# Performance work log

Measured on AMD Instinct MI355X. Metric: run time of the kernel, lower is better.

Reference implementation:

```python
import math
import jax, jax.numpy as jnp
import numpy as np

B, T, N, D, H = 4, 12, 512, 256, 8


def _xavier(key, shape):
    limit = math.sqrt(6.0 / (shape[0] + shape[1]))
    return jax.random.uniform(key, shape, jnp.float32, -limit, limit)


def setup_inputs() -> dict:
    key = jax.random.key(0)
    kx, ks, kq, kk, kv, ko = jax.random.split(key, 6)
    return {
        "x": jax.random.normal(kx, (B, T, N, D), jnp.float32),
        "sim": jax.random.normal(ks, (N, N), jnp.float32),
        "Wq": _xavier(kq, (D, D)),
        "Wk": _xavier(kk, (D, D)),
        "Wv": _xavier(kv, (D, D)),
        "Wo": _xavier(ko, (D, D)),
    }


def reference(x, sim, Wq, Wk, Wv, Wo):
    # x: [B, T, N, D]; attention over spatial dim N, per (batch, time, head).
    b, t, n, d = x.shape
    hd = d // H
    scale = 1.0 / math.sqrt(hd)

    def split_heads(z):  # [B,T,N,D] -> [B,H,T,N,hd]
        return z.reshape(b, t, n, H, hd).transpose(0, 3, 1, 2, 4)

    q = split_heads(x @ Wq)
    k = split_heads(x @ Wk)
    v = split_heads(x @ Wv)

    # scores: [B,H,T,N,N]; additive sim bias broadcast over B,H,T
    scores = jnp.einsum("bhtnd,bhtmd->bhtnm", q, k) * scale + sim
    attn = jax.nn.softmax(scores, axis=-1)  # (dropout p=0.1 omitted: eval mode)
    out = jnp.einsum("bhtnm,bhtmd->bhtnd", attn, v)
    out = out.transpose(0, 2, 3, 1, 4).reshape(b, t, n, d)  # merge heads
    return out @ Wo
```

## Files before the change

### kernel.cpp

```cpp
#include <hip/hip_runtime.h>
#include <hip/hip_bf16.h>

#define BTT 48
#define SEQ 512
#define DIM 256
#define NH  8
#define HD  32
#define QKVD 768

typedef unsigned short u16;
typedef __attribute__((ext_vector_type(8))) short bf16x8;
typedef __attribute__((ext_vector_type(4))) float f32x4;
typedef __attribute__((ext_vector_type(2))) unsigned int u32x2;

__device__ __forceinline__ float fexp2(float x) {
#if __has_builtin(__builtin_amdgcn_exp2f)
  return __builtin_amdgcn_exp2f(x);
#else
  float r; asm("v_exp_f32 %0, %1" : "=v"(r) : "v"(x)); return r;
#endif
}
__device__ __forceinline__ unsigned cvtpk_bf16(float lo, float hi) {
  unsigned r;
  asm("v_cvt_pk_bf16_f32 %0, %1, %2" : "=v"(r) : "v"(lo), "v"(hi));
  return r;
}

__device__ __forceinline__ u16 f2b(float f) {
  __hip_bfloat16 h = __float2bfloat16(f);
  union { __hip_bfloat16 h; u16 u; } c; c.h = h; return c.u;
}
__device__ __forceinline__ bf16x8 ldfrag8(const u16* p) {
  union { uint2 u[2]; bf16x8 v; } f;
  f.u[0] = *reinterpret_cast<const uint2*>(p);
  f.u[1] = *reinterpret_cast<const uint2*>(p + 4);
  return f.v;
}
__device__ __forceinline__ bf16x8 ldfrag16(const u16* p) {
  union { uint4 u; bf16x8 v; } f;
  f.u = *reinterpret_cast<const uint4*>(p);
  return f.v;
}

__global__ __launch_bounds__(256) void wtcvt4_kernel(const float* __restrict__ W0,
                                                     const float* __restrict__ W1,
                                                     const float* __restrict__ W2,
                                                     const float* __restrict__ W3,
                                                     u16* __restrict__ dst, float sc0) {
  __shared__ float Ls[64][65];
  const int z = blockIdx.z;
  const float* W = (z == 0) ? W0 : (z == 1) ? W1 : (z == 2) ? W2 : W3;
  u16* Bt = dst + (size_t)z * DIM * DIM;
  const float sc = (z == 0) ? sc0 : 1.0f;
  const int t = threadIdx.x;
  const int kt = blockIdx.x * 64, nt = blockIdx.y * 64;
#pragma unroll
  for (int it = 0; it < 4; ++it) {
    int r = (t >> 4) + it * 16;
    int c = (t & 15) * 4;
    float4 v = *reinterpret_cast<const float4*>(&W[(size_t)(kt + r) * 256 + nt + c]);
    Ls[r][c] = v.x; Ls[r][c + 1] = v.y; Ls[r][c + 2] = v.z; Ls[r][c + 3] = v.w;
  }
  __syncthreads();
  const int n = t >> 2, kc = (t & 3) * 16;
  union { uint4 u[2]; u16 s[16]; } ob;
#pragma unroll
  for (int j = 0; j < 16; ++j) ob.s[j] = f2b(Ls[kc + j][n] * sc);
  u16* dp = Bt + (size_t)(nt + n) * 256 + kt + kc;
  *reinterpret_cast<uint4*>(dp)     = ob.u[0];
  *reinterpret_cast<uint4*>(dp + 8) = ob.u[1];
}

__global__ __launch_bounds__(256) void simpack_kernel(const float* __restrict__ sim,
                                                      float* __restrict__ simT2) {
  const float LOG2E = 1.4426950408889634f;
  int gid = blockIdx.x * 256 + threadIdx.x;
  int q = gid & 511, k4 = gid >> 9;
  float4 v = *reinterpret_cast<const float4*>(&sim[(size_t)q * 512 + k4 * 4]);
  v.x *= LOG2E; v.y *= LOG2E; v.z *= LOG2E; v.w *= LOG2E;
  *reinterpret_cast<float4*>(&simT2[((size_t)k4 * 512 + q) * 4]) = v;
}

template <typename AIN, typename OUT>
__global__ __launch_bounds__(256) void gemm_mfma(const AIN* __restrict__ A,
                                                 const u16* __restrict__ Bt,
                                                 OUT* __restrict__ C,
                                                 int M, int N, int K) {
  __shared__ u16 As[128][36];
  __shared__ u16 Bs[128][36];
  const int t = threadIdx.x, lane = t & 63, w = t >> 6;
  const int g = lane >> 4, ln = lane & 15;
  const int bm = blockIdx.x * 128, bn = blockIdx.y * 128;
  const int wr = (w & 1) * 64, wc = (w >> 1) * 64;
  const f32x4 zf = {0.f, 0.f, 0.f, 0.f};
  f32x4 acc[4][4];
#pragma unroll
  for (int i = 0; i < 4; ++i)
#pragma unroll
    for (int j = 0; j < 4; ++j) acc[i][j] = zf;

  const int r0 = t >> 2, c8 = (t & 3) * 8;
  uint4 bpre[2];
  float4 apf0[2], apf1[2];
  uint4 apb[2];
#pragma unroll
  for (int p = 0; p < 2; ++p) {
    const size_t arow = (size_t)(bm + r0 + p * 64) * K + c8;
    if constexpr (sizeof(AIN) == 4) {
      apf0[p] = *reinterpret_cast<const float4*>((const float*)A + arow);
      apf1[p] = *reinterpret_cast<const float4*>((const float*)A + arow + 4);
    } else {
      apb[p] = *reinterpret_cast<const uint4*>((const u16*)A + arow);
    }
    bpre[p] = *reinterpret_cast<const uint4*>(&Bt[(size_t)(bn + r0 + p * 64) * K + c8]);
  }

  for (int k0 = 0; k0 < K; k0 += 32) {
#pragma unroll
    for (int p = 0; p < 2; ++p) {
      const int r = r0 + p * 64;
      uint2 a0, a1;
      if constexpr (sizeof(AIN) == 4) {
        a0.x = cvtpk_bf16(apf0[p].x, apf0[p].y);
        a0.y = cvtpk_bf16(apf0[p].z, apf0[p].w);
        a1.x = cvtpk_bf16(apf1[p].x, apf1[p].y);
        a1.y = cvtpk_bf16(apf1[p].z, apf1[p].w);
      } else {
        union { uint4 u4; uint2 u2[2]; } av; av.u4 = apb[p];
        a0 = av.u2[0]; a1 = av.u2[1];
      }
      union { uint4 u4; uint2 u2[2]; } bv; bv.u4 = bpre[p];
      *reinterpret_cast<uint2*>(&As[r][c8])     = a0;
      *reinterpret_cast<uint2*>(&As[r][c8 + 4]) = a1;
      *reinterpret_cast<uint2*>(&Bs[r][c8])     = bv.u2[0];
      *reinterpret_cast<uint2*>(&Bs[r][c8 + 4]) = bv.u2[1];
    }
    if (k0 + 32 < K) {
#pragma unroll
      for (int p = 0; p < 2; ++p) {
        const size_t arow = (size_t)(bm + r0 + p * 64) * K + k0 + 32 + c8;
        if constexpr (sizeof(AIN) == 4) {
          apf0[p] = *reinterpret_cast<const float4*>((const float*)A + arow);
          apf1[p] = *reinterpret_cast<const float4*>((const float*)A + arow + 4);
        } else {
          apb[p] = *reinterpret_cast<const uint4*>((const u16*)A + arow);
        }
        bpre[p] = *reinterpret_cast<const uint4*>(&Bt[(size_t)(bn + r0 + p * 64) * K + k0 + 32 + c8]);
      }
    }
    __syncthreads();
    bf16x8 af[4], bfr[4];
#pragma unroll
    for (int i = 0; i < 4; ++i) af[i]  = ldfrag8(&As[wr + i * 16 + ln][g * 8]);
#pragma unroll
    for (int j = 0; j < 4; ++j) bfr[j] = ldfrag8(&Bs[wc + j * 16 + ln][g * 8]);
#pragma unroll
    for (int i = 0; i < 4; ++i)
#pragma unroll
      for (int j = 0; j < 4; ++j)
        acc[i][j] = __builtin_amdgcn_mfma_f32_16x16x32_bf16(af[i], bfr[j], acc[i][j], 0, 0, 0);
    __syncthreads();
  }
#pragma unroll
  for (int i = 0; i < 4; ++i)
#pragma unroll
    for (int j = 0; j < 4; ++j)
#pragma unroll
      for (int r = 0; r < 4; ++r) {
        const int row = bm + wr + i * 16 + g * 4 + r;
        const int col = bn + wc + j * 16 + ln;
        if constexpr (sizeof(OUT) == 2)
          ((u16*)C)[(size_t)row * N + col] = f2b(acc[i][j][r]);
        else
          ((float*)C)[(size_t)row * N + col] = acc[i][j][r];
      }
}

#define TRRD(dst, base, OFFSTR) \
  asm volatile("ds_read_b64_tr_b16 %0, %1 offset:" OFFSTR : "=v"(dst) : "v"(base))

__global__ __launch_bounds__(256) void attn_mfma10(const u16* __restrict__ QKV,
                                                   const float* __restrict__ simT2,
                                                   u16* __restrict__ O) {
  __shared__ u16 Ks[64][36];
  __shared__ u16 Vn[2][64][16];
  __shared__ u16 Pws[4][2][16][68];

  const int t = threadIdx.x;
  const int lane = t & 63, w = t >> 6;
  const int g = lane >> 4, ln = lane & 15;

  const int flat = blockIdx.x + 4 * (blockIdx.y + 8 * (int)blockIdx.z);
  const int work = (flat & 7) * 192 + (flat >> 3);
  const int qb = work & 3;
  const int grp = work >> 2;
  const int h = grp & 7, bt = grp >> 3;

  const size_t base = (size_t)bt * SEQ * QKVD + (size_t)h * HD;
  const u16* Qp = QKV + base;
  const u16* Kp = QKV + base + 256;
  const u16* Vp = QKV + base + 512;
  const size_t baseo = (size_t)bt * SEQ * DIM + (size_t)h * HD;
  const int wq = qb * 128 + w * 32;

  bf16x8 qf[2];
#pragma unroll
  for (int qt = 0; qt < 2; ++qt)
    qf[qt] = ldfrag16(&Qp[(size_t)(wq + qt * 16 + ln) * QKVD + g * 8]);

  const f32x4 zf = {0.f, 0.f, 0.f, 0.f};
  f32x4 o[2][2];
  float lacc[2];
#pragma unroll
  for (int qt = 0; qt < 2; ++qt) { o[qt][0] = zf; o[qt][1] = zf; lacc[qt] = 0.f; }

  const float4* bq[2];
#pragma unroll
  for (int qt = 0; qt < 2; ++qt)
    bq[qt] = (const float4*)simT2 + ((size_t)g * 512 + (wq + qt * 16 + ln));

  const int sr = t >> 2, sc8 = (t & 3) * 8;
  uint4 kreg = *reinterpret_cast<const uint4*>(&Kp[(size_t)sr * QKVD + sc8]);
  uint4 vreg = *reinterpret_cast<const uint4*>(&Vp[(size_t)sr * QKVD + sc8]);

  const unsigned trbase = (unsigned)(unsigned long long)(&Vn[0][0][0])
                        + (unsigned)(g * 256 + ln * 8);

  for (int it = 0; it < 8; ++it) {
    {
      union { uint4 u4; uint2 u2[2]; } kv;
      kv.u4 = kreg;
      *reinterpret_cast<uint2*>(&Ks[sr][sc8])     = kv.u2[0];
      *reinterpret_cast<uint2*>(&Ks[sr][sc8 + 4]) = kv.u2[1];
      *reinterpret_cast<uint4*>(&Vn[sc8 >> 4][sr][sc8 & 15]) = vreg;
    }
    if (it < 7) {
      const size_t off = (size_t)(it + 1) * 64 * QKVD + (size_t)sr * QKVD + sc8;
      kreg = *reinterpret_cast<const uint4*>(&Kp[off]);
      vreg = *reinterpret_cast<const uint4*>(&Vp[off]);
    }
    __syncthreads();

    float4 bc[2][4];
#pragma unroll
    for (int qt = 0; qt < 2; ++qt)
#pragma unroll
      for (int kt = 0; kt < 4; ++kt)
        bc[qt][kt] = bq[qt][kt * 2048];

    bf16x8 kf[4];
#pragma unroll
    for (int kt = 0; kt < 4; ++kt) kf[kt] = ldfrag8(&Ks[kt * 16 + ln][g * 8]);

    bf16x8 vf[2][2];
    {
      u32x2 r00a, r00b, r01a, r01b, r10a, r10b, r11a, r11b;
      TRRD(r00a, trbase, "0");     TRRD(r00b, trbase, "128");
      TRRD(r01a, trbase, "1024");  TRRD(r01b, trbase, "1152");
      TRRD(r10a, trbase, "2048");  TRRD(r10b, trbase, "2176");
      TRRD(r11a, trbase, "3072");  TRRD(r11b, trbase, "3200");
      asm volatile("s_waitcnt lgkmcnt(0)" ::: "memory");
      __builtin_amdgcn_sched_barrier(0);
      union { u32x2 p[2]; bf16x8 v; } u;
      u.p[0] = r00a; u.p[1] = r00b; vf[0][0] = u.v;
      u.p[0] = r01a; u.p[1] = r01b; vf[0][1] = u.v;
      u.p[0] = r10a; u.p[1] = r10b; vf[1][0] = u.v;
      u.p[0] = r11a; u.p[1] = r11b; vf[1][1] = u.v;
    }

#pragma unroll
    for (int qt = 0; qt < 2; ++qt) {
      f32x4 s[4];
#pragma unroll
      for (int kt = 0; kt < 4; ++kt) {
        const float4 b4 = bc[qt][kt];
        f32x4 ci = {b4.x, b4.y, b4.z, b4.w};
        s[kt] = ci;
      }
      __builtin_amdgcn_s_setprio(1);
#pragma unroll
      for (int kt = 0; kt < 4; ++kt)
        s[kt] = __builtin_amdgcn_mfma_f32_16x16x32_bf16(kf[kt], qf[qt], s[kt], 0, 0, 0);
      __builtin_amdgcn_s_setprio(0);
      bf16x8 pfr[2];
      if (qt > 0) {
#pragma unroll
        for (int ks = 0; ks < 2; ++ks)
          pfr[ks] = ldfrag8(&Pws[w][0][ln][ks * 32 + g * 8]);
      }
      float lsum = 0.f;
#pragma unroll
      for (int kt = 0; kt < 4; ++kt) {
        const float e0 = fexp2(s[kt][0]);
        const float e1 = fexp2(s[kt][1]);
        const float e2 = fexp2(s[kt][2]);
        const float e3 = fexp2(s[kt][3]);
        lsum += (e0 + e1) + (e2 + e3);
        uint2 pw;
        pw.x = cvtpk_bf16(e0, e1);
        pw.y = cvtpk_bf16(e2, e3);
        *reinterpret_cast<uint2*>(&Pws[w][qt][ln][kt * 16 + g * 4]) = pw;
      }
      lacc[qt] += lsum;
      if (qt > 0) {
        __builtin_amdgcn_s_setprio(1);
#pragma unroll
        for (int ks = 0; ks < 2; ++ks)
#pragma unroll
          for (int hf = 0; hf < 2; ++hf)
            o[0][hf] = __builtin_amdgcn_mfma_f32_16x16x32_bf16(pfr[ks], vf[hf][ks], o[0][hf], 0, 0, 0);
        __builtin_amdgcn_s_setprio(0);
      }
    }
    {
      bf16x8 pfr[2];
#pragma unroll
      for (int ks = 0; ks < 2; ++ks)
        pfr[ks] = ldfrag8(&Pws[w][1][ln][ks * 32 + g * 8]);
      __builtin_amdgcn_s_setprio(1);
#pragma unroll
      for (int ks = 0; ks < 2; ++ks)
#pragma unroll
        for (int hf = 0; hf < 2; ++hf)
          o[1][hf] = __builtin_amdgcn_mfma_f32_16x16x32_bf16(pfr[ks], vf[hf][ks], o[1][hf], 0, 0, 0);
      __builtin_amdgcn_s_setprio(0);
    }
#pragma unroll
    for (int qt = 0; qt < 2; ++qt) bq[qt] += 16 * 512;
    __syncthreads();
  }

#pragma unroll
  for (int qt = 0; qt < 2; ++qt) {
    float l = lacc[qt];
    l += __shfl_xor(l, 16);
    l += __shfl_xor(l, 32);
    const float invl = 1.0f / l;
#pragma unroll
    for (int r = 0; r < 4; ++r) {
      const float il = __shfl(invl, g * 4 + r);
      const int qrow = wq + qt * 16 + g * 4 + r;
      O[baseo + (size_t)qrow * DIM + ln]      = f2b(o[qt][0][r] * il);
      O[baseo + (size_t)qrow * DIM + 16 + ln] = f2b(o[qt][1][r] * il);
    }
  }
}

extern "C" void kernel_launch(void* const* d_in, const int* in_sizes, int n_in,
                              void* d_out, int out_size, void* d_ws, size_t ws_size,
                              hipStream_t stream) {
  const float* x   = (const float*)d_in[0];
  const float* sim = (const float*)d_in[1];
  const float* Wq  = (const float*)d_in[2];
  const float* Wk  = (const float*)d_in[3];
  const float* Wv  = (const float*)d_in[4];
  const float* Wo  = (const float*)d_in[5];
  float* out = (float*)d_out;

  const int M = BTT * SEQ;
  const size_t sz = (size_t)M * DIM;
  const int WN = DIM * DIM;
  const float SCALE2 = 0.17677669529663687f * 1.4426950408889634f;

  u16* QKVw  = (u16*)d_ws;
  u16* Aw    = QKVw + (size_t)M * QKVD;
  u16* Wqkvb = Aw + sz;
  u16* Wob   = Wqkvb + (size_t)3 * WN;
  float* simT2 = (float*)(Wob + WN);

  wtcvt4_kernel<<<dim3(4, 4, 4), 256, 0, stream>>>(Wq, Wk, Wv, Wo, Wqkvb, SCALE2);
  simpack_kernel<<<256, 256, 0, stream>>>(sim, simT2);

  gemm_mfma<float, u16><<<dim3(M / 128, QKVD / 128), 256, 0, stream>>>(x, Wqkvb, QKVw, M, QKVD, DIM);

  attn_mfma10<<<dim3(4, NH, BTT), 256, 0, stream>>>(QKVw, simT2, Aw);

  gemm_mfma<u16, float><<<dim3(M / 128, DIM / 128), 256, 0, stream>>>(Aw, Wob, out, M, DIM, DIM);
}
```

Baseline: 80.87 us.

## Double-buffer K/V tiles in attention and swizzle GEMM block order across XCDs

```diff
diff --git a/kernel.cpp b/kernel.cpp
--- a/kernel.cpp
+++ b/kernel.cpp
@@ -90,7 +90,13 @@
   __shared__ u16 Bs[128][36];
   const int t = threadIdx.x, lane = t & 63, w = t >> 6;
   const int g = lane >> 4, ln = lane & 15;
-  const int bm = blockIdx.x * 128, bn = blockIdx.y * 128;
+
+  const int gx = gridDim.x, gy = gridDim.y;
+  const int flat = blockIdx.x + gx * blockIdx.y;
+  const int chunk = (gx * gy) >> 3;
+  const int work = (flat & 7) * chunk + (flat >> 3);
+  const int bm = (work / gy) * 128, bn = (work % gy) * 128;
+
   const int wr = (w & 1) * 64, wc = (w >> 1) * 64;
   const f32x4 zf = {0.f, 0.f, 0.f, 0.f};
   f32x4 acc[4][4];
@@ -179,11 +185,11 @@
 #define TRRD(dst, base, OFFSTR) \
   asm volatile("ds_read_b64_tr_b16 %0, %1 offset:" OFFSTR : "=v"(dst) : "v"(base))
 
-__global__ __launch_bounds__(256) void attn_mfma10(const u16* __restrict__ QKV,
+__global__ __launch_bounds__(256) void attn_mfma11(const u16* __restrict__ QKV,
                                                    const float* __restrict__ simT2,
                                                    u16* __restrict__ O) {
-  __shared__ u16 Ks[64][36];
-  __shared__ u16 Vn[2][64][16];
+  __shared__ u16 Ks[2][64][36];
+  __shared__ u16 Vn[2][2][64][16];
   __shared__ u16 Pws[4][2][16][68];
 
   const int t = threadIdx.x;
@@ -223,16 +229,17 @@
   uint4 kreg = *reinterpret_cast<const uint4*>(&Kp[(size_t)sr * QKVD + sc8]);
   uint4 vreg = *reinterpret_cast<const uint4*>(&Vp[(size_t)sr * QKVD + sc8]);
 
-  const unsigned trbase = (unsigned)(unsigned long long)(&Vn[0][0][0])
-                        + (unsigned)(g * 256 + ln * 8);
+  const unsigned trbase0 = (unsigned)(unsigned long long)(&Vn[0][0][0][0])
+                         + (unsigned)(g * 256 + ln * 8);
 
   for (int it = 0; it < 8; ++it) {
+    const int buf = it & 1;
     {
       union { uint4 u4; uint2 u2[2]; } kv;
       kv.u4 = kreg;
-      *reinterpret_cast<uint2*>(&Ks[sr][sc8])     = kv.u2[0];
-      *reinterpret_cast<uint2*>(&Ks[sr][sc8 + 4]) = kv.u2[1];
-      *reinterpret_cast<uint4*>(&Vn[sc8 >> 4][sr][sc8 & 15]) = vreg;
+      *reinterpret_cast<uint2*>(&Ks[buf][sr][sc8])     = kv.u2[0];
+      *reinterpret_cast<uint2*>(&Ks[buf][sr][sc8 + 4]) = kv.u2[1];
+      *reinterpret_cast<uint4*>(&Vn[buf][sc8 >> 4][sr][sc8 & 15]) = vreg;
     }
     if (it < 7) {
       const size_t off = (size_t)(it + 1) * 64 * QKVD + (size_t)sr * QKVD + sc8;
@@ -250,15 +257,16 @@
 
     bf16x8 kf[4];
 #pragma unroll
-    for (int kt = 0; kt < 4; ++kt) kf[kt] = ldfrag8(&Ks[kt * 16 + ln][g * 8]);
+    for (int kt = 0; kt < 4; ++kt) kf[kt] = ldfrag8(&Ks[buf][kt * 16 + ln][g * 8]);
 
     bf16x8 vf[2][2];
     {
+      const unsigned trb = trbase0 + (unsigned)(buf * 4096);
       u32x2 r00a, r00b, r01a, r01b, r10a, r10b, r11a, r11b;
-      TRRD(r00a, trbase, "0");     TRRD(r00b, trbase, "128");
-      TRRD(r01a, trbase, "1024");  TRRD(r01b, trbase, "1152");
-      TRRD(r10a, trbase, "2048");  TRRD(r10b, trbase, "2176");
-      TRRD(r11a, trbase, "3072");  TRRD(r11b, trbase, "3200");
+      TRRD(r00a, trb, "0");     TRRD(r00b, trb, "128");
+      TRRD(r01a, trb, "1024");  TRRD(r01b, trb, "1152");
+      TRRD(r10a, trb, "2048");  TRRD(r10b, trb, "2176");
+      TRRD(r11a, trb, "3072");  TRRD(r11b, trb, "3200");
       asm volatile("s_waitcnt lgkmcnt(0)" ::: "memory");
       __builtin_amdgcn_sched_barrier(0);
       union { u32x2 p[2]; bf16x8 v; } u;
@@ -327,7 +335,6 @@
     }
 #pragma unroll
     for (int qt = 0; qt < 2; ++qt) bq[qt] += 16 * 512;
-    __syncthreads();
   }
 
 #pragma unroll
@@ -373,7 +380,7 @@
 
   gemm_mfma<float, u16><<<dim3(M / 128, QKVD / 128), 256, 0, stream>>>(x, Wqkvb, QKVw, M, QKVD, DIM);
 
-  attn_mfma10<<<dim3(4, NH, BTT), 256, 0, stream>>>(QKVw, simT2, Aw);
+  attn_mfma11<<<dim3(4, NH, BTT), 256, 0, stream>>>(QKVw, simT2, Aw);
 
   gemm_mfma<u16, float><<<dim3(M / 128, DIM / 128), 256, 0, stream>>>(Aw, Wob, out, M, DIM, DIM);
 }
```

After: 79.30 us. About the same (-1.9%).
